# Optimization experiments

Measured on AMD Instinct MI355X. Metric: run time of the kernel, lower is better.

Reference implementation:

```python
import jax, jax.numpy as jnp
import numpy as np

N, F_IN, H, E, G = 100000, 128, 64, 1600000, 256
BN_EPS = 1e-5


def setup_inputs() -> dict:
    key = jax.random.key(0)
    ks = jax.random.split(key, 32)
    rn = lambda k, shp, s=0.1: jax.random.normal(k, shp, jnp.float32) * s
    ru = lambda k, shp: jax.random.uniform(k, shp, jnp.float32)
    inp = {
        'x': jax.random.normal(ks[0], (N, F_IN), jnp.float32),
        'edge_index': jax.random.randint(ks[1], (2, E), 0, N),
        'batch': jnp.sort(jax.random.randint(ks[2], (N,), 0, G)),
        'w0': rn(ks[3], (F_IN, H)), 'b0': rn(ks[4], (H,)),
        'w1': rn(ks[5], (H, H)), 'b1': rn(ks[6], (H,)),
        'w2': rn(ks[7], (H, H)), 'b2': rn(ks[8], (H,)),
        'g0': ru(ks[9], (H,)) + 0.5, 'beta0': rn(ks[10], (H,)),
        'm0': rn(ks[11], (H,)), 'v0': ru(ks[12], (H,)) + 0.5,
        'g1': ru(ks[13], (H,)) + 0.5, 'beta1': rn(ks[14], (H,)),
        'm1': rn(ks[15], (H,)), 'v1': ru(ks[16], (H,)) + 0.5,
        'g2': ru(ks[17], (H,)) + 0.5, 'beta2': rn(ks[18], (H,)),
        'm2': rn(ks[19], (H,)), 'v2': ru(ks[20], (H,)) + 0.5,
        'l1w': rn(ks[21], (H, H // 2)), 'l1b': rn(ks[22], (H // 2,)),
        'l2w': rn(ks[23], (H // 2, 2)), 'l2b': rn(ks[24], (2,)),
    }
    return inp


def reference(x, edge_index, batch, w0, b0, w1, b1, w2, b2,
              g0, beta0, m0, v0, g1, beta1, m1, v1, g2, beta2, m2, v2,
              l1w, l1b, l2w, l2b):
    n = x.shape[0]
    # GCN: add self-loops, symmetric normalization deg^{-1/2} A_hat deg^{-1/2}
    loop = jnp.arange(n)
    src = jnp.concatenate([edge_index[0], loop])
    dst = jnp.concatenate([edge_index[1], loop])
    deg = jax.ops.segment_sum(jnp.ones_like(src, dtype=x.dtype), dst, num_segments=n)
    dinv = jax.lax.rsqrt(jnp.maximum(deg, 1.0))  # deg >= 1 after self-loops
    norm = (dinv[src] * dinv[dst])[:, None]      # [E+N, 1]

    def gcn(h, w, b):
        h = h @ w                                              # [N, H]
        agg = jax.ops.segment_sum(h[src] * norm, dst, num_segments=n)
        return agg + b

    def bn(h, g, be, m, v):  # eval-mode BatchNorm1d (running stats)
        return (h - m) * (g * jax.lax.rsqrt(v + BN_EPS)) + be

    h = jax.nn.relu(bn(gcn(x, w0, b0), g0, beta0, m0, v0))
    h = jax.nn.relu(bn(gcn(h, w1, b1), g1, beta1, m1, v1))
    h = jax.nn.relu(bn(gcn(h, w2, b2), g2, beta2, m2, v2))
    pooled = jax.ops.segment_sum(h, batch, num_segments=G)     # global_add_pool
    h = jax.nn.relu(pooled @ l1w + l1b)
    return h @ l2w + l2b                                        # [G, 2]
```

## Files before the change

### kernel.cpp

```cpp
#include <hip/hip_runtime.h>
#include <hip/hip_bf16.h>

#define BN_EPS 1e-5f

typedef short bf16x8 __attribute__((ext_vector_type(8)));
typedef float f32x4 __attribute__((ext_vector_type(4)));

static __device__ __forceinline__ unsigned short f2bf(float f) {
    unsigned u = __float_as_uint(f);
    unsigned r = (u + 0x7FFF + ((u >> 16) & 1)) >> 16;
    return (unsigned short)r;
}
static __device__ __forceinline__ float bf2f(unsigned short s) {
    return __uint_as_float((unsigned)s << 16);
}
__device__ __forceinline__ int pad8i(int c) { return (c + 7) & ~7; }

#define BIN_SHIFT 9
#define BIN_NODES 512
#define P1_CHUNK 8192
#define IMG_CAP 12288

#define SCAN_CHUNK 1024

__global__ void scan_block_sums(const int* __restrict__ cnt, int* __restrict__ bsums, int n) {
    __shared__ int sdata[256];
    int b = blockIdx.x, t = threadIdx.x;
    int base = b * SCAN_CHUNK;
    int s = 0;
    for (int i = t; i < SCAN_CHUNK; i += 256) {
        int idx = base + i;
        if (idx < n) s += pad8i(cnt[idx]);
    }
    sdata[t] = s;
    __syncthreads();
    for (int off = 128; off > 0; off >>= 1) {
        if (t < off) sdata[t] += sdata[t + off];
        __syncthreads();
    }
    if (t == 0) bsums[b] = sdata[0];
}

__global__ void scan_exclusive_bsums(int* __restrict__ bsums, int nb) {
    if (threadIdx.x == 0 && blockIdx.x == 0) {
        int acc = 0;
        for (int i = 0; i < nb; i++) { int v = bsums[i]; bsums[i] = acc; acc += v; }
    }
}

__global__ void scan_write(const int* __restrict__ cnt, const int* __restrict__ bsums,
                           int* __restrict__ row_start, int n) {
    __shared__ int sdata[256];
    int b = blockIdx.x, t = threadIdx.x;
    int base = b * SCAN_CHUNK + t * 4;
    int v0 = 0, v1 = 0, v2 = 0, v3 = 0;
    if (base + 0 < n) v0 = pad8i(cnt[base + 0]);
    if (base + 1 < n) v1 = pad8i(cnt[base + 1]);
    if (base + 2 < n) v2 = pad8i(cnt[base + 2]);
    if (base + 3 < n) v3 = pad8i(cnt[base + 3]);
    int tsum = v0 + v1 + v2 + v3;
    sdata[t] = tsum;
    __syncthreads();
    for (int off = 1; off < 256; off <<= 1) {
        int x = (t >= off) ? sdata[t - off] : 0;
        __syncthreads();
        sdata[t] += x;
        __syncthreads();
    }
    int excl = sdata[t] - tsum + bsums[b];
    if (base + 0 < n) row_start[base + 0] = excl;
    if (base + 1 < n) row_start[base + 1] = excl + v0;
    if (base + 2 < n) row_start[base + 2] = excl + v0 + v1;
    if (base + 3 < n) row_start[base + 3] = excl + v0 + v1 + v2;
    if (n - 1 >= base && n - 1 < base + 4)
        row_start[n] = excl + v0 + v1 + v2 + v3;
}

__global__ __launch_bounds__(256) void binhist_kernel(const int* __restrict__ dst,
                                                      int* __restrict__ bincnt,
                                                      int e, int nbins) {
    __shared__ int hist[256];
    int t = threadIdx.x;
    hist[t] = 0;
    __syncthreads();
    int c0 = blockIdx.x * P1_CHUNK;
    int iend = c0 + P1_CHUNK; if (iend > e) iend = e;
    for (int i = c0 + t; i < iend; i += 256)
        atomicAdd(&hist[dst[i] >> BIN_SHIFT], 1);
    __syncthreads();
    if (t < nbins && hist[t] > 0) atomicAdd(&bincnt[t], hist[t]);
}

__global__ void scan_small(const int* __restrict__ in, int* __restrict__ out, int m) {
    if (threadIdx.x == 0 && blockIdx.x == 0) {
        int a = 0;
        for (int i = 0; i < m; i++) { out[i] = a; a += in[i]; }
        out[m] = a;
    }
}

__global__ __launch_bounds__(256) void phase1_kernel(
        const int* __restrict__ src, const int* __restrict__ dst,
        const int* __restrict__ bstart_e, int* __restrict__ bincur,
        int* __restrict__ ebuf, int e, int nbins) {
    __shared__ int hist[256], base[256], cur[256];
    int t = threadIdx.x;
    int c0 = blockIdx.x * P1_CHUNK;
    int iend = c0 + P1_CHUNK; if (iend > e) iend = e;
    hist[t] = 0;
    __syncthreads();
    for (int i = c0 + t; i < iend; i += 256)
        atomicAdd(&hist[dst[i] >> BIN_SHIFT], 1);
    __syncthreads();
    if (t < nbins && hist[t] > 0)
        base[t] = bstart_e[t] + atomicAdd(&bincur[t], hist[t]);
    cur[t] = 0;
    __syncthreads();
    for (int i = c0 + t; i < iend; i += 256) {
        int s = src[i], d = dst[i];
        int b = d >> BIN_SHIFT;
        int r = atomicAdd(&cur[b], 1);
        ebuf[base[b] + r] = s | ((d & (BIN_NODES - 1)) << 17);
    }
}

__global__ __launch_bounds__(256) void bincount_kernel(
        const int* __restrict__ ebuf, const int* __restrict__ bstart_e,
        int* __restrict__ cnt, float* __restrict__ dinv, int n) {
    __shared__ int c512[BIN_NODES];
    int b = blockIdx.x, t = threadIdx.x;
    for (int k = t; k < BIN_NODES; k += 256) c512[k] = 0;
    __syncthreads();
    int e0 = bstart_e[b], e1 = bstart_e[b + 1];
    for (int j = e0 + t; j < e1; j += 256)
        atomicAdd(&c512[ebuf[j] >> 17], 1);
    __syncthreads();
    int n0 = b * BIN_NODES;
    for (int k = t; k < BIN_NODES; k += 256) {
        int i = n0 + k;
        if (i < n) {
            int c = c512[k];
            cnt[i] = c;
            dinv[i] = rsqrtf((float)(c + 1));
        }
    }
}

__global__ __launch_bounds__(256) void phase2_kernel(
        const int* __restrict__ ebuf, const int* __restrict__ bstart_e,
        const int* __restrict__ row_start, int* __restrict__ csr,
        int* __restrict__ gcursor, int n, int sentinel) {
    __shared__ int image[IMG_CAP];
    __shared__ int lcur[BIN_NODES];
    int b = blockIdx.x, t = threadIdx.x;
    int n0 = b * BIN_NODES;
    int n1 = n0 + BIN_NODES; if (n1 > n) n1 = n;
    int rbase = row_start[n0];
    int rspan = row_start[n1] - rbase;
    int e0 = bstart_e[b], e1 = bstart_e[b + 1];
    for (int k = t; k < BIN_NODES; k += 256) lcur[k] = 0;
    if (rspan <= IMG_CAP) {
        for (int k = t; k < rspan; k += 256) image[k] = sentinel;
        __syncthreads();
        for (int j = e0 + t; j < e1; j += 256) {
            int en = ebuf[j];
            int s = en & 0x1FFFF;
            int dl = en >> 17;
            int pos = row_start[n0 + dl] - rbase + atomicAdd(&lcur[dl], 1);
            image[pos] = s;
        }
        __syncthreads();
        for (int k = t; k < rspan; k += 256) csr[rbase + k] = image[k];
    } else {
        __syncthreads();
        for (int j = e0 + t; j < e1; j += 256) {
            int en = ebuf[j];
            int s = en & 0x1FFFF;
            int dl = en >> 17;
            int pos = row_start[n0 + dl] + atomicAdd(&gcursor[n0 + dl], 1);
            csr[pos] = s;
        }
        __syncthreads();
        for (int k = t; k < n1 - n0; k += 256) {
            int node = n0 + k;
            int c = gcursor[node];
            for (int pos = row_start[node] + c; pos < row_start[node + 1]; pos++)
                csr[pos] = sentinel;
        }
    }
}

template<int K, bool BF16IN>
__global__ __launch_bounds__(256) void lin_mfma(const void* __restrict__ in_,
                                                const float* __restrict__ w,
                                                const float* __restrict__ dinv,
                                                unsigned short* __restrict__ outbf, int n) {
    constexpr int XS = K + 8;
    __shared__ unsigned short xs[64 * XS];
    __shared__ unsigned short wt[64 * XS];
    int t = threadIdx.x;
    int row0 = blockIdx.x * 64;
    int nrows = n - row0; if (nrows > 64) nrows = 64;

    {
        const float4* w4 = (const float4*)w;
        for (int idx = t; idx < K * 16; idx += 256) {
            int k = idx >> 4, c4 = (idx & 15) * 4;
            float4 v = w4[idx];
            wt[(c4 + 0) * XS + k] = f2bf(v.x);
            wt[(c4 + 1) * XS + k] = f2bf(v.y);
            wt[(c4 + 2) * XS + k] = f2bf(v.z);
            wt[(c4 + 3) * XS + k] = f2bf(v.w);
        }
    }
    if constexpr (BF16IN) {
        const uint4* in4 = (const uint4*)((const unsigned short*)in_ + (size_t)row0 * K);
        int total8 = nrows * (K / 8);
        for (int idx = t; idx < total8; idx += 256) {
            int r = idx / (K / 8), kk = idx - r * (K / 8);
            uint4 v = in4[idx];
            *(uint4*)&xs[r * XS + kk * 8] = v;
        }
    } else {
        const float4* in4 = (const float4*)((const float*)in_ + (size_t)row0 * K);
        int total4 = nrows * (K / 4);
        for (int idx = t; idx < total4; idx += 256) {
            int r = idx / (K / 4), kk = idx - r * (K / 4);
            float4 v = in4[idx];
            ushort4 s4;
            s4.x = f2bf(v.x); s4.y = f2bf(v.y); s4.z = f2bf(v.z); s4.w = f2bf(v.w);
            *(ushort4*)&xs[r * XS + kk * 4] = s4;
        }
    }
    __syncthreads();

    int lane = t & 63;
    int wid = t >> 6;
    int quad = lane >> 4;
    int l15 = lane & 15;

    f32x4 acc[4];
#pragma unroll
    for (int cg = 0; cg < 4; cg++) acc[cg] = (f32x4){0.f, 0.f, 0.f, 0.f};

    const unsigned short* xrow = &xs[(wid * 16 + l15) * XS + quad * 8];
#pragma unroll
    for (int kc = 0; kc < K / 32; kc++) {
        bf16x8 bfrag = *(const bf16x8*)(xrow + kc * 32);
#pragma unroll
        for (int cg = 0; cg < 4; cg++) {
            bf16x8 afrag = *(const bf16x8*)&wt[(cg * 16 + l15) * XS + kc * 32 + quad * 8];
            acc[cg] = __builtin_amdgcn_mfma_f32_16x16x32_bf16(afrag, bfrag, acc[cg], 0, 0, 0);
        }
    }

    int grow = row0 + wid * 16 + l15;
    if (grow < n) {
        float dv = dinv[grow];
#pragma unroll
        for (int cg = 0; cg < 4; cg++) {
            ushort4 st;
            st.x = f2bf(acc[cg][0] * dv);
            st.y = f2bf(acc[cg][1] * dv);
            st.z = f2bf(acc[cg][2] * dv);
            st.w = f2bf(acc[cg][3] * dv);
            *(ushort4*)&outbf[(size_t)grow * 64 + cg * 16 + quad * 4] = st;
        }
    }
}

__global__ __launch_bounds__(256) void agg_kernel(
        const unsigned short* __restrict__ hs, const int* __restrict__ row_start,
        const int* __restrict__ csr, const float* __restrict__ dinv,
        const float* __restrict__ bias, const float* __restrict__ gam,
        const float* __restrict__ bet, const float* __restrict__ mu,
        const float* __restrict__ var,
        unsigned short* __restrict__ out, int n) {
    int i = blockIdx.x * 4 + (threadIdx.x >> 6);
    int lane = threadIdx.x & 63;
    if (i >= n) return;
    float acc = bf2f(hs[(size_t)i * 64 + lane]);
    int rs = row_start[i], re = row_start[i + 1];
    int j = rs;
    for (; j + 16 <= re; j += 16) {
        int4 c0 = *(const int4*)&csr[j];
        int4 c1 = *(const int4*)&csr[j + 4];
        int4 c2 = *(const int4*)&csr[j + 8];
        int4 c3 = *(const int4*)&csr[j + 12];
        float h0 = bf2f(hs[(size_t)c0.x * 64 + lane]);
        float h1 = bf2f(hs[(size_t)c0.y * 64 + lane]);
        float h2 = bf2f(hs[(size_t)c0.z * 64 + lane]);
        float h3 = bf2f(hs[(size_t)c0.w * 64 + lane]);
        float h4 = bf2f(hs[(size_t)c1.x * 64 + lane]);
        float h5 = bf2f(hs[(size_t)c1.y * 64 + lane]);
        float h6 = bf2f(hs[(size_t)c1.z * 64 + lane]);
        float h7 = bf2f(hs[(size_t)c1.w * 64 + lane]);
        float h8 = bf2f(hs[(size_t)c2.x * 64 + lane]);
        float h9 = bf2f(hs[(size_t)c2.y * 64 + lane]);
        float hA = bf2f(hs[(size_t)c2.z * 64 + lane]);
        float hB = bf2f(hs[(size_t)c2.w * 64 + lane]);
        float hC = bf2f(hs[(size_t)c3.x * 64 + lane]);
        float hD = bf2f(hs[(size_t)c3.y * 64 + lane]);
        float hE = bf2f(hs[(size_t)c3.z * 64 + lane]);
        float hF = bf2f(hs[(size_t)c3.w * 64 + lane]);
        acc += (((h0 + h1) + (h2 + h3)) + ((h4 + h5) + (h6 + h7)))
             + (((h8 + h9) + (hA + hB)) + ((hC + hD) + (hE + hF)));
    }
    for (; j < re; j += 8) {
        int4 c0 = *(const int4*)&csr[j];
        int4 c1 = *(const int4*)&csr[j + 4];
        float h0 = bf2f(hs[(size_t)c0.x * 64 + lane]);
        float h1 = bf2f(hs[(size_t)c0.y * 64 + lane]);
        float h2 = bf2f(hs[(size_t)c0.z * 64 + lane]);
        float h3 = bf2f(hs[(size_t)c0.w * 64 + lane]);
        float h4 = bf2f(hs[(size_t)c1.x * 64 + lane]);
        float h5 = bf2f(hs[(size_t)c1.y * 64 + lane]);
        float h6 = bf2f(hs[(size_t)c1.z * 64 + lane]);
        float h7 = bf2f(hs[(size_t)c1.w * 64 + lane]);
        acc += ((h0 + h1) + (h2 + h3)) + ((h4 + h5) + (h6 + h7));
    }
    float agg = acc * dinv[i];
    float scale = gam[lane] * rsqrtf(var[lane] + BN_EPS);
    float r = (agg + bias[lane] - mu[lane]) * scale + bet[lane];
    out[(size_t)i * 64 + lane] = f2bf(r > 0.f ? r : 0.f);
}

#define POOL_CHUNK 64
__global__ __launch_bounds__(256) void pool_kernel(const unsigned short* __restrict__ h,
                                                   const int* __restrict__ batch,
                                                   float* __restrict__ pooled, int n) {
    int wid = blockIdx.x * 4 + (threadIdx.x >> 6);
    int lane = threadIdx.x & 63;
    int start = wid * POOL_CHUNK;
    if (start >= n) return;
    int end = start + POOL_CHUNK; if (end > n) end = n;
    int cur = batch[start];
    float acc = 0.f;
    for (int i = start; i < end; i++) {
        int b = batch[i];
        if (b != cur) {
            atomicAdd(&pooled[(size_t)cur * 64 + lane], acc);
            acc = 0.f; cur = b;
        }
        acc += bf2f(h[(size_t)i * 64 + lane]);
    }
    atomicAdd(&pooled[(size_t)cur * 64 + lane], acc);
}

__global__ void mlp_kernel(const float* __restrict__ pooled,
                           const float* __restrict__ l1w, const float* __restrict__ l1b,
                           const float* __restrict__ l2w, const float* __restrict__ l2b,
                           float* __restrict__ out) {
    int g = blockIdx.x;
    int lane = threadIdx.x;
    __shared__ float p[64];
    __shared__ float h1[32];
    p[lane] = pooled[(size_t)g * 64 + lane];
    __syncthreads();
    if (lane < 32) {
        float a = l1b[lane];
#pragma unroll 8
        for (int k = 0; k < 64; k++) a += p[k] * l1w[k * 32 + lane];
        h1[lane] = a > 0.f ? a : 0.f;
    }
    __syncthreads();
    if (lane < 2) {
        float a = l2b[lane];
#pragma unroll 8
        for (int j = 0; j < 32; j++) a += h1[j] * l2w[j * 2 + lane];
        out[g * 2 + lane] = a;
    }
}

extern "C" void kernel_launch(void* const* d_in, const int* in_sizes, int n_in,
                              void* d_out, int out_size, void* d_ws, size_t ws_size,
                              hipStream_t stream) {
    const float* x     = (const float*)d_in[0];
    const int*   ei    = (const int*)d_in[1];
    const int*   batch = (const int*)d_in[2];
    const float* w0 = (const float*)d_in[3];
    const float* b0 = (const float*)d_in[4];
    const float* w1 = (const float*)d_in[5];
    const float* b1 = (const float*)d_in[6];
    const float* w2 = (const float*)d_in[7];
    const float* b2 = (const float*)d_in[8];
    const float* g0 = (const float*)d_in[9];
    const float* be0 = (const float*)d_in[10];
    const float* m0 = (const float*)d_in[11];
    const float* v0 = (const float*)d_in[12];
    const float* g1 = (const float*)d_in[13];
    const float* be1 = (const float*)d_in[14];
    const float* m1 = (const float*)d_in[15];
    const float* v1 = (const float*)d_in[16];
    const float* g2 = (const float*)d_in[17];
    const float* be2 = (const float*)d_in[18];
    const float* m2 = (const float*)d_in[19];
    const float* v2 = (const float*)d_in[20];
    const float* l1w = (const float*)d_in[21];
    const float* l1b = (const float*)d_in[22];
    const float* l2w = (const float*)d_in[23];
    const float* l2b = (const float*)d_in[24];
    float* out = (float*)d_out;

    const int N = in_sizes[2];
    const int E = in_sizes[1] / 2;
    const int G = out_size / 2;
    const int NBINS = (N + BIN_NODES - 1) / BIN_NODES;

    const int* src = ei;
    const int* dst = ei + E;

    char* p = (char*)d_ws;
    auto alloc = [&](size_t bytes) -> void* {
        void* r = (void*)p;
        p += (bytes + 255) & ~(size_t)255;
        return r;
    };
    const size_t CSR_CAP = ((size_t)E + 8 * (size_t)N + 3) & ~(size_t)3;
    float* dinvp    = (float*)alloc((size_t)N * 4);
    int*   cnt      = (int*)alloc((size_t)N * 4);
    int*   row_start= (int*)alloc((size_t)(N + 1) * 4);
    int*   cursor   = (int*)alloc((size_t)N * 4);
    int    NB       = (N + SCAN_CHUNK - 1) / SCAN_CHUNK;
    int*   bsums    = (int*)alloc((size_t)NB * 4);
    int*   bincnt   = (int*)alloc((size_t)NBINS * 4);
    int*   bstart_e = (int*)alloc((size_t)(NBINS + 1) * 4);
    int*   bincur   = (int*)alloc((size_t)NBINS * 4);
    int*   ebuf     = (int*)alloc((size_t)E * 4);
    int*   csr      = (int*)alloc(CSR_CAP * 4);
    unsigned short* h_a = (unsigned short*)alloc((size_t)(N + 1) * 64 * 2);
    unsigned short* h_b = (unsigned short*)alloc((size_t)N * 64 * 2);
    float* pooled   = (float*)alloc((size_t)G * 64 * 4);
    (void)ws_size;

    hipMemsetAsync(cursor, 0, (size_t)N * 4, stream);
    hipMemsetAsync(bincnt, 0, (size_t)NBINS * 4, stream);
    hipMemsetAsync(bincur, 0, (size_t)NBINS * 4, stream);
    hipMemsetAsync(pooled, 0, (size_t)G * 64 * 4, stream);
    hipMemsetAsync(h_a + (size_t)N * 64, 0, 64 * 2, stream);
    const int nchunks = (E + P1_CHUNK - 1) / P1_CHUNK;
    binhist_kernel<<<nchunks, 256, 0, stream>>>(dst, bincnt, E, NBINS);
    scan_small<<<1, 64, 0, stream>>>(bincnt, bstart_e, NBINS);
    phase1_kernel<<<nchunks, 256, 0, stream>>>(src, dst, bstart_e, bincur, ebuf, E, NBINS);
    bincount_kernel<<<NBINS, 256, 0, stream>>>(ebuf, bstart_e, cnt, dinvp, N);
    scan_block_sums<<<NB, 256, 0, stream>>>(cnt, bsums, N);
    scan_exclusive_bsums<<<1, 64, 0, stream>>>(bsums, NB);
    scan_write<<<NB, 256, 0, stream>>>(cnt, bsums, row_start, N);
    phase2_kernel<<<NBINS, 256, 0, stream>>>(ebuf, bstart_e, row_start, csr,
                                             cursor, N, N);

    const int nblk = (N + 3) / 4;
    const int lblk = (N + 63) / 64;
    lin_mfma<128, false><<<lblk, 256, 0, stream>>>(x, w0, dinvp, h_a, N);
    agg_kernel<<<nblk, 256, 0, stream>>>(h_a, row_start, csr, dinvp,
                                         b0, g0, be0, m0, v0, h_b, N);
    lin_mfma<64, true><<<lblk, 256, 0, stream>>>(h_b, w1, dinvp, h_a, N);
    agg_kernel<<<nblk, 256, 0, stream>>>(h_a, row_start, csr, dinvp,
                                         b1, g1, be1, m1, v1, h_b, N);
    lin_mfma<64, true><<<lblk, 256, 0, stream>>>(h_b, w2, dinvp, h_a, N);
    agg_kernel<<<nblk, 256, 0, stream>>>(h_a, row_start, csr, dinvp,
                                         b2, g2, be2, m2, v2, h_b, N);
    const int pwaves = (N + POOL_CHUNK - 1) / POOL_CHUNK;
    pool_kernel<<<(pwaves + 3) / 4, 256, 0, stream>>>(h_b, batch, pooled, N);
    mlp_kernel<<<G, 64, 0, stream>>>(pooled, l1w, l1b, l2w, l2b, out);
}
```

Baseline: 420.6 us.

## Fuse CSR preprocessing into one cooperative kernel and fuse pooling into last aggregation

```diff
diff --git a/kernel.cpp b/kernel.cpp
--- a/kernel.cpp
+++ b/kernel.cpp
@@ -1,5 +1,8 @@
 #include <hip/hip_runtime.h>
 #include <hip/hip_bf16.h>
+#include <hip/hip_cooperative_groups.h>
+
+namespace cg = cooperative_groups;
 
 #define BN_EPS 1e-5f
 
@@ -20,173 +23,183 @@
 #define BIN_NODES 512
 #define P1_CHUNK 8192
 #define IMG_CAP 12288
-
 #define SCAN_CHUNK 1024
-
-__global__ void scan_block_sums(const int* __restrict__ cnt, int* __restrict__ bsums, int n) {
-    __shared__ int sdata[256];
-    int b = blockIdx.x, t = threadIdx.x;
-    int base = b * SCAN_CHUNK;
-    int s = 0;
-    for (int i = t; i < SCAN_CHUNK; i += 256) {
-        int idx = base + i;
-        if (idx < n) s += pad8i(cnt[idx]);
-    }
-    sdata[t] = s;
-    __syncthreads();
-    for (int off = 128; off > 0; off >>= 1) {
-        if (t < off) sdata[t] += sdata[t + off];
-        __syncthreads();
-    }
-    if (t == 0) bsums[b] = sdata[0];
-}
-
-__global__ void scan_exclusive_bsums(int* __restrict__ bsums, int nb) {
-    if (threadIdx.x == 0 && blockIdx.x == 0) {
+#define COOP_GRID 512
+
+struct PreArgs {
+    const int* src; const int* dst; int e;
+    int* bincnt; int* bstart_e; int* bincur; int* ebuf;
+    int* cnt; float* dinv; int* bsums; int* row_start; int* csr; int* cursor;
+    unsigned short* ha_sent; float* pooled;
+    int n; int nbins; int nb; int gpool;
+};
+
+__global__ __launch_bounds__(256) void preprocess_coop(PreArgs a) {
+    cg::grid_group grid = cg::this_grid();
+    __shared__ int smem[IMG_CAP + BIN_NODES];
+    int t = threadIdx.x, blk = blockIdx.x, nblk = gridDim.x;
+    int gtid = blk * 256 + t, gstride = nblk * 256;
+
+    for (int i = gtid; i < a.nbins; i += gstride) { a.bincnt[i] = 0; a.bincur[i] = 0; }
+    for (int i = gtid; i < a.n; i += gstride) a.cursor[i] = 0;
+    for (int i = gtid; i < a.gpool * 64; i += gstride) a.pooled[i] = 0.f;
+    if (gtid < 64) a.ha_sent[gtid] = 0;
+    grid.sync();
+
+    int nchunks = (a.e + P1_CHUNK - 1) / P1_CHUNK;
+    for (int c = blk; c < nchunks; c += nblk) {
+        int* hist = smem;
+        hist[t] = 0;
+        __syncthreads();
+        int c0 = c * P1_CHUNK, iend = min(c0 + P1_CHUNK, a.e);
+        for (int i = c0 + t; i < iend; i += 256)
+            atomicAdd(&hist[a.dst[i] >> BIN_SHIFT], 1);
+        __syncthreads();
+        if (t < a.nbins && hist[t] > 0) atomicAdd(&a.bincnt[t], hist[t]);
+        __syncthreads();
+    }
+    grid.sync();
+
+    if (blk == 0 && t == 0) {
         int acc = 0;
-        for (int i = 0; i < nb; i++) { int v = bsums[i]; bsums[i] = acc; acc += v; }
-    }
-}
-
-__global__ void scan_write(const int* __restrict__ cnt, const int* __restrict__ bsums,
-                           int* __restrict__ row_start, int n) {
-    __shared__ int sdata[256];
-    int b = blockIdx.x, t = threadIdx.x;
-    int base = b * SCAN_CHUNK + t * 4;
-    int v0 = 0, v1 = 0, v2 = 0, v3 = 0;
-    if (base + 0 < n) v0 = pad8i(cnt[base + 0]);
-    if (base + 1 < n) v1 = pad8i(cnt[base + 1]);
-    if (base + 2 < n) v2 = pad8i(cnt[base + 2]);
-    if (base + 3 < n) v3 = pad8i(cnt[base + 3]);
-    int tsum = v0 + v1 + v2 + v3;
-    sdata[t] = tsum;
-    __syncthreads();
-    for (int off = 1; off < 256; off <<= 1) {
-        int x = (t >= off) ? sdata[t - off] : 0;
-        __syncthreads();
-        sdata[t] += x;
-        __syncthreads();
-    }
-    int excl = sdata[t] - tsum + bsums[b];
-    if (base + 0 < n) row_start[base + 0] = excl;
-    if (base + 1 < n) row_start[base + 1] = excl + v0;
-    if (base + 2 < n) row_start[base + 2] = excl + v0 + v1;
-    if (base + 3 < n) row_start[base + 3] = excl + v0 + v1 + v2;
-    if (n - 1 >= base && n - 1 < base + 4)
-        row_start[n] = excl + v0 + v1 + v2 + v3;
-}
-
-__global__ __launch_bounds__(256) void binhist_kernel(const int* __restrict__ dst,
-                                                      int* __restrict__ bincnt,
-                                                      int e, int nbins) {
-    __shared__ int hist[256];
-    int t = threadIdx.x;
-    hist[t] = 0;
-    __syncthreads();
-    int c0 = blockIdx.x * P1_CHUNK;
-    int iend = c0 + P1_CHUNK; if (iend > e) iend = e;
-    for (int i = c0 + t; i < iend; i += 256)
-        atomicAdd(&hist[dst[i] >> BIN_SHIFT], 1);
-    __syncthreads();
-    if (t < nbins && hist[t] > 0) atomicAdd(&bincnt[t], hist[t]);
-}
-
-__global__ void scan_small(const int* __restrict__ in, int* __restrict__ out, int m) {
-    if (threadIdx.x == 0 && blockIdx.x == 0) {
-        int a = 0;
-        for (int i = 0; i < m; i++) { out[i] = a; a += in[i]; }
-        out[m] = a;
-    }
-}
-
-__global__ __launch_bounds__(256) void phase1_kernel(
-        const int* __restrict__ src, const int* __restrict__ dst,
-        const int* __restrict__ bstart_e, int* __restrict__ bincur,
-        int* __restrict__ ebuf, int e, int nbins) {
-    __shared__ int hist[256], base[256], cur[256];
-    int t = threadIdx.x;
-    int c0 = blockIdx.x * P1_CHUNK;
-    int iend = c0 + P1_CHUNK; if (iend > e) iend = e;
-    hist[t] = 0;
-    __syncthreads();
-    for (int i = c0 + t; i < iend; i += 256)
-        atomicAdd(&hist[dst[i] >> BIN_SHIFT], 1);
-    __syncthreads();
-    if (t < nbins && hist[t] > 0)
-        base[t] = bstart_e[t] + atomicAdd(&bincur[t], hist[t]);
-    cur[t] = 0;
-    __syncthreads();
-    for (int i = c0 + t; i < iend; i += 256) {
-        int s = src[i], d = dst[i];
-        int b = d >> BIN_SHIFT;
-        int r = atomicAdd(&cur[b], 1);
-        ebuf[base[b] + r] = s | ((d & (BIN_NODES - 1)) << 17);
-    }
-}
-
-__global__ __launch_bounds__(256) void bincount_kernel(
-        const int* __restrict__ ebuf, const int* __restrict__ bstart_e,
-        int* __restrict__ cnt, float* __restrict__ dinv, int n) {
-    __shared__ int c512[BIN_NODES];
-    int b = blockIdx.x, t = threadIdx.x;
-    for (int k = t; k < BIN_NODES; k += 256) c512[k] = 0;
-    __syncthreads();
-    int e0 = bstart_e[b], e1 = bstart_e[b + 1];
-    for (int j = e0 + t; j < e1; j += 256)
-        atomicAdd(&c512[ebuf[j] >> 17], 1);
-    __syncthreads();
-    int n0 = b * BIN_NODES;
-    for (int k = t; k < BIN_NODES; k += 256) {
-        int i = n0 + k;
-        if (i < n) {
-            int c = c512[k];
-            cnt[i] = c;
-            dinv[i] = rsqrtf((float)(c + 1));
-        }
-    }
-}
-
-__global__ __launch_bounds__(256) void phase2_kernel(
-        const int* __restrict__ ebuf, const int* __restrict__ bstart_e,
-        const int* __restrict__ row_start, int* __restrict__ csr,
-        int* __restrict__ gcursor, int n, int sentinel) {
-    __shared__ int image[IMG_CAP];
-    __shared__ int lcur[BIN_NODES];
-    int b = blockIdx.x, t = threadIdx.x;
-    int n0 = b * BIN_NODES;
-    int n1 = n0 + BIN_NODES; if (n1 > n) n1 = n;
-    int rbase = row_start[n0];
-    int rspan = row_start[n1] - rbase;
-    int e0 = bstart_e[b], e1 = bstart_e[b + 1];
-    for (int k = t; k < BIN_NODES; k += 256) lcur[k] = 0;
-    if (rspan <= IMG_CAP) {
-        for (int k = t; k < rspan; k += 256) image[k] = sentinel;
-        __syncthreads();
-        for (int j = e0 + t; j < e1; j += 256) {
-            int en = ebuf[j];
-            int s = en & 0x1FFFF;
-            int dl = en >> 17;
-            int pos = row_start[n0 + dl] - rbase + atomicAdd(&lcur[dl], 1);
-            image[pos] = s;
-        }
-        __syncthreads();
-        for (int k = t; k < rspan; k += 256) csr[rbase + k] = image[k];
-    } else {
-        __syncthreads();
-        for (int j = e0 + t; j < e1; j += 256) {
-            int en = ebuf[j];
-            int s = en & 0x1FFFF;
-            int dl = en >> 17;
-            int pos = row_start[n0 + dl] + atomicAdd(&gcursor[n0 + dl], 1);
-            csr[pos] = s;
-        }
-        __syncthreads();
-        for (int k = t; k < n1 - n0; k += 256) {
-            int node = n0 + k;
-            int c = gcursor[node];
-            for (int pos = row_start[node] + c; pos < row_start[node + 1]; pos++)
-                csr[pos] = sentinel;
-        }
+        for (int i = 0; i < a.nbins; i++) { a.bstart_e[i] = acc; acc += a.bincnt[i]; }
+        a.bstart_e[a.nbins] = acc;
+    }
+    grid.sync();
+
+    for (int c = blk; c < nchunks; c += nblk) {
+        int* hist = smem; int* base = smem + 256; int* cur = smem + 512;
+        hist[t] = 0;
+        __syncthreads();
+        int c0 = c * P1_CHUNK, iend = min(c0 + P1_CHUNK, a.e);
+        for (int i = c0 + t; i < iend; i += 256)
+            atomicAdd(&hist[a.dst[i] >> BIN_SHIFT], 1);
+        __syncthreads();
+        if (t < a.nbins && hist[t] > 0)
+            base[t] = a.bstart_e[t] + atomicAdd(&a.bincur[t], hist[t]);
+        cur[t] = 0;
+        __syncthreads();
+        for (int i = c0 + t; i < iend; i += 256) {
+            int s = a.src[i], d = a.dst[i];
+            int b = d >> BIN_SHIFT;
+            int r = atomicAdd(&cur[b], 1);
+            a.ebuf[base[b] + r] = s | ((d & (BIN_NODES - 1)) << 17);
+        }
+        __syncthreads();
+    }
+    grid.sync();
+
+    for (int b = blk; b < a.nbins; b += nblk) {
+        int* c512 = smem;
+        for (int k = t; k < BIN_NODES; k += 256) c512[k] = 0;
+        __syncthreads();
+        int e0 = a.bstart_e[b], e1 = a.bstart_e[b + 1];
+        for (int j = e0 + t; j < e1; j += 256)
+            atomicAdd(&c512[a.ebuf[j] >> 17], 1);
+        __syncthreads();
+        int n0 = b * BIN_NODES;
+        for (int k = t; k < BIN_NODES; k += 256) {
+            int i = n0 + k;
+            if (i < a.n) {
+                int c = c512[k];
+                a.cnt[i] = c;
+                a.dinv[i] = rsqrtf((float)(c + 1));
+            }
+        }
+        __syncthreads();
+    }
+    grid.sync();
+
+    for (int b = blk; b < a.nb; b += nblk) {
+        int* sd = smem;
+        int base0 = b * SCAN_CHUNK;
+        int s = 0;
+        for (int i = t; i < SCAN_CHUNK; i += 256) {
+            int idx = base0 + i;
+            if (idx < a.n) s += pad8i(a.cnt[idx]);
+        }
+        sd[t] = s;
+        __syncthreads();
+        for (int off = 128; off > 0; off >>= 1) {
+            if (t < off) sd[t] += sd[t + off];
+            __syncthreads();
+        }
+        if (t == 0) a.bsums[b] = sd[0];
+        __syncthreads();
+    }
+    grid.sync();
+    if (blk == 0 && t == 0) {
+        int acc = 0;
+        for (int i = 0; i < a.nb; i++) { int v = a.bsums[i]; a.bsums[i] = acc; acc += v; }
+    }
+    grid.sync();
+    for (int b = blk; b < a.nb; b += nblk) {
+        int* sd = smem;
+        int base0 = b * SCAN_CHUNK + t * 4;
+        int v0 = 0, v1 = 0, v2 = 0, v3 = 0;
+        if (base0 + 0 < a.n) v0 = pad8i(a.cnt[base0 + 0]);
+        if (base0 + 1 < a.n) v1 = pad8i(a.cnt[base0 + 1]);
+        if (base0 + 2 < a.n) v2 = pad8i(a.cnt[base0 + 2]);
+        if (base0 + 3 < a.n) v3 = pad8i(a.cnt[base0 + 3]);
+        int tsum = v0 + v1 + v2 + v3;
+        sd[t] = tsum;
+        __syncthreads();
+        for (int off = 1; off < 256; off <<= 1) {
+            int x = (t >= off) ? sd[t - off] : 0;
+            __syncthreads();
+            sd[t] += x;
+            __syncthreads();
+        }
+        int excl = sd[t] - tsum + a.bsums[b];
+        if (base0 + 0 < a.n) a.row_start[base0 + 0] = excl;
+        if (base0 + 1 < a.n) a.row_start[base0 + 1] = excl + v0;
+        if (base0 + 2 < a.n) a.row_start[base0 + 2] = excl + v0 + v1;
+        if (base0 + 3 < a.n) a.row_start[base0 + 3] = excl + v0 + v1 + v2;
+        if (a.n - 1 >= base0 && a.n - 1 < base0 + 4)
+            a.row_start[a.n] = excl + v0 + v1 + v2 + v3;
+        __syncthreads();
+    }
+    grid.sync();
+
+    for (int b = blk; b < a.nbins; b += nblk) {
+        int* image = smem; int* lcur = smem + IMG_CAP;
+        __syncthreads();
+        int n0 = b * BIN_NODES;
+        int n1 = min(n0 + BIN_NODES, a.n);
+        int rbase = a.row_start[n0];
+        int rspan = a.row_start[n1] - rbase;
+        int e0 = a.bstart_e[b], e1 = a.bstart_e[b + 1];
+        for (int k = t; k < BIN_NODES; k += 256) lcur[k] = 0;
+        if (rspan <= IMG_CAP) {
+            for (int k = t; k < rspan; k += 256) image[k] = a.n;
+            __syncthreads();
+            for (int j = e0 + t; j < e1; j += 256) {
+                int en = a.ebuf[j];
+                int s = en & 0x1FFFF;
+                int dl = en >> 17;
+                int pos = a.row_start[n0 + dl] - rbase + atomicAdd(&lcur[dl], 1);
+                image[pos] = s;
+            }
+            __syncthreads();
+            for (int k = t; k < rspan; k += 256) a.csr[rbase + k] = image[k];
+        } else {
+            __syncthreads();
+            for (int j = e0 + t; j < e1; j += 256) {
+                int en = a.ebuf[j];
+                int s = en & 0x1FFFF;
+                int dl = en >> 17;
+                int pos = a.row_start[n0 + dl] + atomicAdd(&a.cursor[n0 + dl], 1);
+                a.csr[pos] = s;
+            }
+            __syncthreads();
+            for (int k = t; k < n1 - n0; k += 256) {
+                int node = n0 + k;
+                int c = a.cursor[node];
+                for (int pos = a.row_start[node] + c; pos < a.row_start[node + 1]; pos++)
+                    a.csr[pos] = a.n;
+            }
+        }
+        __syncthreads();
     }
 }
 
@@ -241,16 +254,16 @@
 
     f32x4 acc[4];
 #pragma unroll
-    for (int cg = 0; cg < 4; cg++) acc[cg] = (f32x4){0.f, 0.f, 0.f, 0.f};
+    for (int cg_ = 0; cg_ < 4; cg_++) acc[cg_] = (f32x4){0.f, 0.f, 0.f, 0.f};
 
     const unsigned short* xrow = &xs[(wid * 16 + l15) * XS + quad * 8];
 #pragma unroll
     for (int kc = 0; kc < K / 32; kc++) {
         bf16x8 bfrag = *(const bf16x8*)(xrow + kc * 32);
 #pragma unroll
-        for (int cg = 0; cg < 4; cg++) {
-            bf16x8 afrag = *(const bf16x8*)&wt[(cg * 16 + l15) * XS + kc * 32 + quad * 8];
-            acc[cg] = __builtin_amdgcn_mfma_f32_16x16x32_bf16(afrag, bfrag, acc[cg], 0, 0, 0);
+        for (int cg_ = 0; cg_ < 4; cg_++) {
+            bf16x8 afrag = *(const bf16x8*)&wt[(cg_ * 16 + l15) * XS + kc * 32 + quad * 8];
+            acc[cg_] = __builtin_amdgcn_mfma_f32_16x16x32_bf16(afrag, bfrag, acc[cg_], 0, 0, 0);
         }
     }
 
@@ -258,24 +271,26 @@
     if (grow < n) {
         float dv = dinv[grow];
 #pragma unroll
-        for (int cg = 0; cg < 4; cg++) {
+        for (int cg_ = 0; cg_ < 4; cg_++) {
             ushort4 st;
-            st.x = f2bf(acc[cg][0] * dv);
-            st.y = f2bf(acc[cg][1] * dv);
-            st.z = f2bf(acc[cg][2] * dv);
-            st.w = f2bf(acc[cg][3] * dv);
-            *(ushort4*)&outbf[(size_t)grow * 64 + cg * 16 + quad * 4] = st;
-        }
-    }
-}
-
+            st.x = f2bf(acc[cg_][0] * dv);
+            st.y = f2bf(acc[cg_][1] * dv);
+            st.z = f2bf(acc[cg_][2] * dv);
+            st.w = f2bf(acc[cg_][3] * dv);
+            *(ushort4*)&outbf[(size_t)grow * 64 + cg_ * 16 + quad * 4] = st;
+        }
+    }
+}
+
+template<bool FUSE_POOL>
 __global__ __launch_bounds__(256) void agg_kernel(
         const unsigned short* __restrict__ hs, const int* __restrict__ row_start,
         const int* __restrict__ csr, const float* __restrict__ dinv,
         const float* __restrict__ bias, const float* __restrict__ gam,
         const float* __restrict__ bet, const float* __restrict__ mu,
         const float* __restrict__ var,
-        unsigned short* __restrict__ out, int n) {
+        unsigned short* __restrict__ out, const int* __restrict__ batch,
+        float* __restrict__ pooled, int n) {
     int i = blockIdx.x * 4 + (threadIdx.x >> 6);
     int lane = threadIdx.x & 63;
     if (i >= n) return;
@@ -322,29 +337,13 @@
     float agg = acc * dinv[i];
     float scale = gam[lane] * rsqrtf(var[lane] + BN_EPS);
     float r = (agg + bias[lane] - mu[lane]) * scale + bet[lane];
-    out[(size_t)i * 64 + lane] = f2bf(r > 0.f ? r : 0.f);
-}
-
-#define POOL_CHUNK 64
-__global__ __launch_bounds__(256) void pool_kernel(const unsigned short* __restrict__ h,
-                                                   const int* __restrict__ batch,
-                                                   float* __restrict__ pooled, int n) {
-    int wid = blockIdx.x * 4 + (threadIdx.x >> 6);
-    int lane = threadIdx.x & 63;
-    int start = wid * POOL_CHUNK;
-    if (start >= n) return;
-    int end = start + POOL_CHUNK; if (end > n) end = n;
-    int cur = batch[start];
-    float acc = 0.f;
-    for (int i = start; i < end; i++) {
-        int b = batch[i];
-        if (b != cur) {
-            atomicAdd(&pooled[(size_t)cur * 64 + lane], acc);
-            acc = 0.f; cur = b;
-        }
-        acc += bf2f(h[(size_t)i * 64 + lane]);
-    }
-    atomicAdd(&pooled[(size_t)cur * 64 + lane], acc);
+    r = r > 0.f ? r : 0.f;
+    if constexpr (FUSE_POOL) {
+        int g = batch[i];
+        atomicAdd(&pooled[(size_t)g * 64 + lane], r);
+    } else {
+        out[(size_t)i * 64 + lane] = f2bf(r);
+    }
 }
 
 __global__ void mlp_kernel(const float* __restrict__ pooled,
@@ -406,6 +405,7 @@
     const int E = in_sizes[1] / 2;
     const int G = out_size / 2;
     const int NBINS = (N + BIN_NODES - 1) / BIN_NODES;
+    const int NB = (N + SCAN_CHUNK - 1) / SCAN_CHUNK;
 
     const int* src = ei;
     const int* dst = ei + E;
@@ -421,7 +421,6 @@
     int*   cnt      = (int*)alloc((size_t)N * 4);
     int*   row_start= (int*)alloc((size_t)(N + 1) * 4);
     int*   cursor   = (int*)alloc((size_t)N * 4);
-    int    NB       = (N + SCAN_CHUNK - 1) / SCAN_CHUNK;
     int*   bsums    = (int*)alloc((size_t)NB * 4);
     int*   bincnt   = (int*)alloc((size_t)NBINS * 4);
     int*   bstart_e = (int*)alloc((size_t)(NBINS + 1) * 4);
@@ -433,34 +432,30 @@
     float* pooled   = (float*)alloc((size_t)G * 64 * 4);
     (void)ws_size;
 
-    hipMemsetAsync(cursor, 0, (size_t)N * 4, stream);
-    hipMemsetAsync(bincnt, 0, (size_t)NBINS * 4, stream);
-    hipMemsetAsync(bincur, 0, (size_t)NBINS * 4, stream);
-    hipMemsetAsync(pooled, 0, (size_t)G * 64 * 4, stream);
-    hipMemsetAsync(h_a + (size_t)N * 64, 0, 64 * 2, stream);
-    const int nchunks = (E + P1_CHUNK - 1) / P1_CHUNK;
-    binhist_kernel<<<nchunks, 256, 0, stream>>>(dst, bincnt, E, NBINS);
-    scan_small<<<1, 64, 0, stream>>>(bincnt, bstart_e, NBINS);
-    phase1_kernel<<<nchunks, 256, 0, stream>>>(src, dst, bstart_e, bincur, ebuf, E, NBINS);
-    bincount_kernel<<<NBINS, 256, 0, stream>>>(ebuf, bstart_e, cnt, dinvp, N);
-    scan_block_sums<<<NB, 256, 0, stream>>>(cnt, bsums, N);
-    scan_exclusive_bsums<<<1, 64, 0, stream>>>(bsums, NB);
-    scan_write<<<NB, 256, 0, stream>>>(cnt, bsums, row_start, N);
-    phase2_kernel<<<NBINS, 256, 0, stream>>>(ebuf, bstart_e, row_start, csr,
-                                             cursor, N, N);
+    PreArgs pa;
+    pa.src = src; pa.dst = dst; pa.e = E;
+    pa.bincnt = bincnt; pa.bstart_e = bstart_e; pa.bincur = bincur; pa.ebuf = ebuf;
+    pa.cnt = cnt; pa.dinv = dinvp; pa.bsums = bsums; pa.row_start = row_start;
+    pa.csr = csr; pa.cursor = cursor;
+    pa.ha_sent = h_a + (size_t)N * 64; pa.pooled = pooled;
+    pa.n = N; pa.nbins = NBINS; pa.nb = NB; pa.gpool = G;
+    void* kargs[] = { (void*)&pa };
+    hipLaunchCooperativeKernel((void*)preprocess_coop, dim3(COOP_GRID), dim3(256),
+                               kargs, 0, stream);
 
     const int nblk = (N + 3) / 4;
     const int lblk = (N + 63) / 64;
     lin_mfma<128, false><<<lblk, 256, 0, stream>>>(x, w0, dinvp, h_a, N);
-    agg_kernel<<<nblk, 256, 0, stream>>>(h_a, row_start, csr, dinvp,
-                                         b0, g0, be0, m0, v0, h_b, N);
+    agg_kernel<false><<<nblk, 256, 0, stream>>>(h_a, row_start, csr, dinvp,
+                                                b0, g0, be0, m0, v0, h_b,
+                                                nullptr, nullptr, N);
     lin_mfma<64, true><<<lblk, 256, 0, stream>>>(h_b, w1, dinvp, h_a, N);
-    agg_kernel<<<nblk, 256, 0, stream>>>(h_a, row_start, csr, dinvp,
-                                         b1, g1, be1, m1, v1, h_b, N);
+    agg_kernel<false><<<nblk, 256, 0, stream>>>(h_a, row_start, csr, dinvp,
+                                                b1, g1, be1, m1, v1, h_b,
+                                                nullptr, nullptr, N);
     lin_mfma<64, true><<<lblk, 256, 0, stream>>>(h_b, w2, dinvp, h_a, N);
-    agg_kernel<<<nblk, 256, 0, stream>>>(h_a, row_start, csr, dinvp,
-                                         b2, g2, be2, m2, v2, h_b, N);
-    const int pwaves = (N + POOL_CHUNK - 1) / POOL_CHUNK;
-    pool_kernel<<<(pwaves + 3) / 4, 256, 0, stream>>>(h_b, batch, pooled, N);
+    agg_kernel<true><<<nblk, 256, 0, stream>>>(h_a, row_start, csr, dinvp,
+                                               b2, g2, be2, m2, v2, nullptr,
+                                               batch, pooled, N);
     mlp_kernel<<<G, 64, 0, stream>>>(pooled, l1w, l1b, l2w, l2b, out);
 }
```

Result: slower. 869.6 us (+106.8%).
